# Performance work log

Hardware: AMD Instinct MI355X
Metric: run time of the kernel (lower is better)

The kernel has to match this reference:

```python
import jax, jax.numpy as jnp
import numpy as np

N_NODES = 50000
IN_DIM = 128
HID = 2 * IN_DIM  # 256, per module: hidden_dim = input_dims * 2
FC1 = 1024
FC2 = 512
N_ACT = 64
N_EDGES = 800000
N_AGENTS = 16384


def _layernorm(h, g, b, eps=1e-5):
    mu = jnp.mean(h, axis=-1, keepdims=True)
    var = jnp.var(h, axis=-1, keepdims=True)
    return (h - mu) * jax.lax.rsqrt(var + eps) * g + b


def setup_inputs() -> dict:
    key = jax.random.key(0)
    ks = jax.random.split(key, 16)
    def u(k, shape, fan_in):
        s = 1.0 / np.sqrt(fan_in)
        return jax.random.uniform(k, shape, jnp.float32, -s, s)
    inp = {}
    inp["x"] = jax.random.normal(ks[0], (N_NODES, IN_DIM), jnp.float32)
    inp["action"] = jax.random.normal(ks[1], (N_AGENTS, N_ACT), jnp.float32)
    inp["edge_index"] = jax.random.randint(ks[2], (2, N_EDGES), 0, N_NODES, jnp.int32)
    inp["agent_idx"] = jax.random.randint(ks[3], (N_AGENTS,), 0, N_NODES, jnp.int32)
    # GCNConv params (linear no bias + separate bias)
    inp["W_gcn"] = u(ks[4], (IN_DIM, HID), IN_DIM)
    inp["b_gcn"] = jnp.zeros((HID,), jnp.float32)
    # fc1, fc2 (custom uniform init per module)
    inp["W1"] = u(ks[5], (HID, FC1), FC1)
    inp["b1"] = u(ks[6], (FC1,), FC1)
    inp["g1"] = jnp.ones((FC1,), jnp.float32)
    inp["beta1"] = jnp.zeros((FC1,), jnp.float32)
    inp["W2"] = u(ks[7], (FC1, FC2), FC2)
    inp["b2"] = u(ks[8], (FC2,), FC2)
    inp["g2"] = jnp.ones((FC2,), jnp.float32)
    inp["beta2"] = jnp.zeros((FC2,), jnp.float32)
    inp["Wa"] = u(ks[9], (N_ACT, FC2), FC2)
    inp["ba"] = u(ks[10], (FC2,), FC2)
    inp["Wq"] = jax.random.uniform(ks[11], (FC2, 1), jnp.float32, -0.003, 0.003)
    inp["bq"] = jax.random.uniform(ks[12], (1,), jnp.float32, -0.003, 0.003)
    return inp


def reference(x, action, W_gcn, b_gcn, W1, b1, g1, beta1, W2, b2, g2, beta2, Wa, ba, Wq, bq, edge_index, agent_idx):
    N = x.shape[0]
    # GCNConv: add self-loops, symmetric D^-1/2 (A+I) D^-1/2 normalization
    loops = jnp.arange(N, dtype=edge_index.dtype)
    src = jnp.concatenate([edge_index[0], loops])
    dst = jnp.concatenate([edge_index[1], loops])
    h = x @ W_gcn  # [N, HID] transform before aggregation
    deg = jax.ops.segment_sum(jnp.ones_like(dst, dtype=h.dtype), dst, num_segments=N)
    dinv = jax.lax.rsqrt(jnp.maximum(deg, 1.0))  # deg >= 1 due to self-loops
    norm = dinv[src] * dinv[dst]  # [E+N]
    agg = jax.ops.segment_sum(h[src] * norm[:, None], dst, num_segments=N) + b_gcn
    # masked gather of agent nodes, then critic MLP
    z = jax.nn.relu(agg[agent_idx])  # [A, HID]
    s = jax.nn.relu(_layernorm(z @ W1 + b1, g1, beta1))
    s = _layernorm(s @ W2 + b2, g2, beta2)
    a = action @ Wa + ba
    sa = jax.nn.relu(s + a)
    return sa @ Wq + bq  # [A, 1]
```

## Files before the change

### kernel.cpp

```cpp
#include <hip/hip_runtime.h>
#include <hip/hip_bf16.h>

typedef _Float16 f16;
typedef _Float16 __attribute__((ext_vector_type(8))) half8;
typedef _Float16 __attribute__((ext_vector_type(4))) half4;
typedef float __attribute__((ext_vector_type(4))) floatx4;

#define IN_DIM 128
#define HID    256
#define FC1    1024
#define FC2    512
#define NACT   64
#define BUCKET 128

__global__ void prep0_kernel(int* degcnt, int* needed, int* n_needed, int* cursor, int N, int A) {
    int b = blockIdx.x, tid = threadIdx.x;
    if (b < 196) {
        int i = b * 256 + tid;
        if (i < N) { degcnt[i] = 0; needed[i] = 0; }
        if (b == 0 && tid == 0) *n_needed = 0;
        return;
    }
    b -= 196;
    cursor[b * 256 + tid] = 0;
}

__device__ __forceinline__ void transpose_tile(const float* __restrict__ in, f16* __restrict__ out,
                                               int K, int N, int bx, int by, int tid) {
    __shared__ f16 tile[32][33];
    int k0 = bx * 32, n0 = by * 32;
    int tx = tid & 31, ty = tid >> 5;
    #pragma unroll
    for (int i = 0; i < 4; ++i)
        tile[ty + i * 8][tx] = (f16)in[(size_t)(k0 + ty + i * 8) * N + n0 + tx];
    __syncthreads();
    #pragma unroll
    for (int i = 0; i < 4; ++i)
        out[(size_t)(n0 + ty + i * 8) * K + k0 + tx] = tile[tx][ty + i * 8];
}

__device__ __forceinline__ void cvt8(const float* __restrict__ in, f16* __restrict__ out, long gi) {
    float4 a = *(const float4*)&in[gi * 8];
    float4 b = *(const float4*)&in[gi * 8 + 4];
    half8 pk;
    pk[0] = (f16)a.x; pk[1] = (f16)a.y; pk[2] = (f16)a.z; pk[3] = (f16)a.w;
    pk[4] = (f16)b.x; pk[5] = (f16)b.y; pk[6] = (f16)b.z; pk[7] = (f16)b.w;
    *(half8*)&out[gi * 8] = pk;
}

__global__ __launch_bounds__(256)
void prep1_kernel(const float* __restrict__ Wgcn, const float* __restrict__ W1,
                  const float* __restrict__ W2, const float* __restrict__ Wa,
                  const float* __restrict__ action, const int* __restrict__ agent_idx,
                  f16* WgcnT, f16* W1T, f16* W2T, f16* WaT, f16* act16,
                  int* needed, int* needed_list, int* n_needed, int A) {
    int b = blockIdx.x, tid = threadIdx.x;
    if (b < 32)  { transpose_tile(Wgcn, WgcnT, IN_DIM, HID, b & 3, b >> 2, tid); return; }
    b -= 32;
    if (b < 256) { transpose_tile(W1, W1T, HID, FC1, b & 7, b >> 3, tid); return; }
    b -= 256;
    if (b < 512) { transpose_tile(W2, W2T, FC1, FC2, b & 31, b >> 5, tid); return; }
    b -= 512;
    if (b < 32)  { transpose_tile(Wa, WaT, NACT, FC2, b & 1, b >> 1, tid); return; }
    b -= 32;
    if (b < 512) { cvt8(action, act16, (long)b * 256 + tid); return; }
    b -= 512;
    int i = b * 256 + tid;
    if (i < A) {
        int idx = agent_idx[i];
        if (atomicCAS(&needed[idx], 0, -1) == 0) {
            int p = atomicAdd(n_needed, 1);
            needed_list[p] = idx;
            needed[idx] = p + 1;
        }
    }
}

__device__ __forceinline__ void swz_decode(int bid, int log2ny, int& bx, int& by) {
    int xcd = bid & 7;
    int pos = bid >> 3;
    bx = (pos >> log2ny) * 8 + xcd;
    by = pos & ((1 << log2ny) - 1);
}

template<bool RELU, bool LIMIT>
__device__ __forceinline__ void gemm_tile64(f16* __restrict__ smA, f16* __restrict__ smB,
                                            const f16* __restrict__ A, const f16* __restrict__ BT,
                                            f16* __restrict__ C, const float* __restrict__ bias,
                                            const int* __restrict__ limit,
                                            int bx, int by, int N, int K) {
    if (LIMIT && bx * 64 >= *limit) return;
    const int tid = threadIdx.x;
    const int lane = tid & 63;
    const int wave = tid >> 6;
    const int wr = wave >> 1, wc = wave & 1;
    const long bm = (long)bx * 64, bn = (long)by * 64;

    size_t aoff[2], boff[2];
    #pragma unroll
    for (int t = 0; t < 2; ++t) {
        int ci = t * 256 + tid;
        int r = ci >> 3, s = ci & 7, ks = s ^ (r & 7);
        aoff[t] = (size_t)(bm + r) * K + ks * 8;
        boff[t] = (size_t)(bn + r) * K + ks * 8;
    }
    int aidx[2][2], bidx[2][2];
    const int kc = lane >> 4;
    #pragma unroll
    for (int kk = 0; kk < 2; ++kk) {
        #pragma unroll
        for (int i = 0; i < 2; ++i) {
            int ar = wr * 32 + i * 16 + (lane & 15);
            aidx[kk][i] = ar * 64 + ((kk * 4 + kc) ^ (ar & 7)) * 8;
            int br = wc * 32 + i * 16 + (lane & 15);
            bidx[kk][i] = br * 64 + ((kk * 4 + kc) ^ (br & 7)) * 8;
        }
    }

    const int NT = K >> 6;
    auto stage = [&](int buf, int k0) {
        #pragma unroll
        for (int t = 0; t < 2; ++t) {
            __builtin_amdgcn_global_load_lds(
                (const __attribute__((address_space(1))) void*)(A + aoff[t] + k0),
                (__attribute__((address_space(3))) void*)(&smA[buf * 4096 + (t * 256 + tid) * 8]), 16, 0, 0);
            __builtin_amdgcn_global_load_lds(
                (const __attribute__((address_space(1))) void*)(BT + boff[t] + k0),
                (__attribute__((address_space(3))) void*)(&smB[buf * 4096 + (t * 256 + tid) * 8]), 16, 0, 0);
        }
    };

    floatx4 acc[2][2] = {};
    stage(0, 0);
    asm volatile("s_waitcnt vmcnt(0)" ::: "memory");
    __builtin_amdgcn_s_barrier();
    int cur = 0;
    for (int t = 0; t < NT; ++t) {
        if (t + 1 < NT) stage(cur ^ 1, (t + 1) << 6);
        #pragma unroll
        for (int kk = 0; kk < 2; ++kk) {
            half8 af[2], bf[2];
            #pragma unroll
            for (int i = 0; i < 2; ++i) {
                af[i] = *(const half8*)&smA[cur * 4096 + aidx[kk][i]];
                bf[i] = *(const half8*)&smB[cur * 4096 + bidx[kk][i]];
            }
            #pragma unroll
            for (int mi = 0; mi < 2; ++mi)
                #pragma unroll
                for (int ni = 0; ni < 2; ++ni)
                    acc[mi][ni] = __builtin_amdgcn_mfma_f32_16x16x32_f16(af[mi], bf[ni], acc[mi][ni], 0, 0, 0);
        }
        asm volatile("s_waitcnt vmcnt(0)" ::: "memory");
        __builtin_amdgcn_s_barrier();
        cur ^= 1;
    }
    f16* scr = smA + wave * 512;
    #pragma unroll
    for (int mi = 0; mi < 2; ++mi) {
        __syncthreads();
        #pragma unroll
        for (int ni = 0; ni < 2; ++ni) {
            int c = ni * 16 + (lane & 15);
            float bz = bias[bn + wc * 32 + c];
            #pragma unroll
            for (int q = 0; q < 4; ++q) {
                int r = (lane >> 4) * 4 + q;
                float v = acc[mi][ni][q] + bz;
                if (RELU) v = fmaxf(v, 0.f);
                scr[r * 32 + c] = (f16)v;
            }
        }
        __syncthreads();
        int r = lane >> 2, ch = lane & 3;
        half8 v = *(const half8*)&scr[r * 32 + ch * 8];
        *(half8*)&C[(size_t)(bm + wr * 32 + mi * 16 + r) * N + (bn + wc * 32 + ch * 8)] = v;
    }
}

template<bool RELU, bool LIMIT>
__global__ __launch_bounds__(256)
void gemm64_kernel(const f16* __restrict__ A, const f16* __restrict__ BT,
                   f16* __restrict__ C, const float* __restrict__ bias,
                   const int* __restrict__ limit, int N, int K, int log2ny) {
    __shared__ __align__(16) f16 smA[2 * 4096];
    __shared__ __align__(16) f16 smB[2 * 4096];
    int bx, by;
    swz_decode(blockIdx.x, log2ny, bx, by);
    gemm_tile64<RELU, LIMIT>(smA, smB, A, BT, C, bias, limit, bx, by, N, K);
}

__global__ __launch_bounds__(256)
void degfill_abuf_kernel(const int* __restrict__ esrc, const int* __restrict__ edst,
                         const int* __restrict__ needed, int* __restrict__ degcnt,
                         int* __restrict__ cursor, int* __restrict__ srcbuf,
                         const f16* __restrict__ act16, const f16* __restrict__ WaT,
                         f16* __restrict__ abuf, const float* __restrict__ ba,
                         int E, int gblk) {
    __shared__ __align__(16) f16 smA[2 * 4096];
    __shared__ __align__(16) f16 smB[2 * 4096];
    int b = blockIdx.x;
    if (b < gblk) {
        int bx, by;
        swz_decode(b, 3, bx, by);
        gemm_tile64<false, false>(smA, smB, act16, WaT, abuf, ba, nullptr, bx, by, FC2, NACT);
        return;
    }
    int e = (b - gblk) * 256 + threadIdx.x;
    if (e < E) {
        int d = edst[e];
        int s = needed[d];
        if (s == 0) {
            atomicAdd(&degcnt[d], 1);
        } else {
            int slot = s - 1;
            int pos = atomicAdd(&cursor[slot], 1);
            if (pos < BUCKET) srcbuf[(size_t)slot * BUCKET + pos] = esrc[e];
        }
    }
}

__global__ __launch_bounds__(256)
void gather_x_kernel(const int* __restrict__ needed_list, const int* __restrict__ n_needed,
                     const int* __restrict__ needed, const int* __restrict__ degcnt,
                     const int* __restrict__ cursor, const int* __restrict__ srcbuf,
                     const float* __restrict__ x, f16* __restrict__ xagg) {
    int w = (blockIdx.x * 256 + threadIdx.x) >> 6;
    int lane = threadIdx.x & 63;
    if (w >= *n_needed) return;
    int d = needed_list[w];
    int degd = cursor[w];
    float dd = rsqrtf((float)degd + 1.0f);
    size_t beg = (size_t)w * BUCKET;
    int cnt = degd < BUCKET ? degd : BUCKET;
    float2 xs = *(const float2*)&x[(size_t)d * IN_DIM + lane * 2];
    float ax = xs.x * dd * dd, ay = xs.y * dd * dd;
    auto src_deg = [&](int s) -> float {
        int ns = needed[s];
        int dg = (ns != 0) ? cursor[ns - 1] : degcnt[s];
        return (float)dg;
    };
    int j = 0;
    for (; j + 3 < cnt; j += 4) {
        int s0 = srcbuf[beg + j], s1 = srcbuf[beg + j + 1];
        int s2 = srcbuf[beg + j + 2], s3 = srcbuf[beg + j + 3];
        float n0 = rsqrtf(src_deg(s0) + 1.0f) * dd;
        float n1 = rsqrtf(src_deg(s1) + 1.0f) * dd;
        float n2 = rsqrtf(src_deg(s2) + 1.0f) * dd;
        float n3 = rsqrtf(src_deg(s3) + 1.0f) * dd;
        float2 v0 = *(const float2*)&x[(size_t)s0 * IN_DIM + lane * 2];
        float2 v1 = *(const float2*)&x[(size_t)s1 * IN_DIM + lane * 2];
        float2 v2 = *(const float2*)&x[(size_t)s2 * IN_DIM + lane * 2];
        float2 v3 = *(const float2*)&x[(size_t)s3 * IN_DIM + lane * 2];
        ax = fmaf(v0.x, n0, ax); ay = fmaf(v0.y, n0, ay);
        ax = fmaf(v1.x, n1, ax); ay = fmaf(v1.y, n1, ay);
        ax = fmaf(v2.x, n2, ax); ay = fmaf(v2.y, n2, ay);
        ax = fmaf(v3.x, n3, ax); ay = fmaf(v3.y, n3, ay);
    }
    for (; j < cnt; ++j) {
        int s0 = srcbuf[beg + j];
        float n0 = rsqrtf(src_deg(s0) + 1.0f) * dd;
        float2 v0 = *(const float2*)&x[(size_t)s0 * IN_DIM + lane * 2];
        ax = fmaf(v0.x, n0, ax);
        ay = fmaf(v0.y, n0, ay);
    }
    union { f16 h[2]; unsigned u; } pk;
    pk.h[0] = (f16)ax; pk.h[1] = (f16)ay;
    *(unsigned*)&xagg[(size_t)w * IN_DIM + lane * 2] = pk.u;
}

template<bool LIMIT>
__device__ __forceinline__ void gemm_tile128(f16* __restrict__ smA, f16* __restrict__ smB,
                                             const f16* __restrict__ A, const f16* __restrict__ BT,
                                             f16* __restrict__ C, const float* __restrict__ bias,
                                             const int* __restrict__ limit,
                                             int bx, int by, int N, int K) {
    if (LIMIT && bx * 128 >= *limit) return;
    const int tid = threadIdx.x;
    const int lane = tid & 63;
    const int wave = tid >> 6;
    const int wr = wave >> 1, wc = wave & 1;
    const long bm = (long)bx * 128, bn = (long)by * 128;

    size_t aoff[4], boff[4];
    #pragma unroll
    for (int t = 0; t < 4; ++t) {
        int ci = t * 256 + tid;
        int r = ci >> 3, s = ci & 7, ks = s ^ (r & 7);
        aoff[t] = (size_t)(bm + r) * K + ks * 8;
        boff[t] = (size_t)(bn + r) * K + ks * 8;
    }
    int aidx[2][4], bidx[2][4];
    const int kc = lane >> 4;
    #pragma unroll
    for (int kk = 0; kk < 2; ++kk) {
        #pragma unroll
        for (int i = 0; i < 4; ++i) {
            int ar = wr * 64 + i * 16 + (lane & 15);
            aidx[kk][i] = ar * 64 + ((kk * 4 + kc) ^ (ar & 7)) * 8;
            int br = wc * 64 + i * 16 + (lane & 15);
            bidx[kk][i] = br * 64 + ((kk * 4 + kc) ^ (br & 7)) * 8;
        }
    }

    const int NT = K >> 6;
    auto stage = [&](int buf, int k0) {
        #pragma unroll
        for (int t = 0; t < 4; ++t) {
            __builtin_amdgcn_global_load_lds(
                (const __attribute__((address_space(1))) void*)(A + aoff[t] + k0),
                (__attribute__((address_space(3))) void*)(&smA[buf * 8192 + (t * 256 + tid) * 8]), 16, 0, 0);
            __builtin_amdgcn_global_load_lds(
                (const __attribute__((address_space(1))) void*)(BT + boff[t] + k0),
                (__attribute__((address_space(3))) void*)(&smB[buf * 8192 + (t * 256 + tid) * 8]), 16, 0, 0);
        }
    };

    floatx4 acc[4][4] = {};
    stage(0, 0);
    asm volatile("s_waitcnt vmcnt(0)" ::: "memory");
    __builtin_amdgcn_s_barrier();
    int cur = 0;
    for (int t = 0; t < NT; ++t) {
        if (t + 1 < NT) stage(cur ^ 1, (t + 1) << 6);
        #pragma unroll
        for (int kk = 0; kk < 2; ++kk) {
            half8 af[4], bf[4];
            #pragma unroll
            for (int i = 0; i < 4; ++i) {
                af[i] = *(const half8*)&smA[cur * 8192 + aidx[kk][i]];
                bf[i] = *(const half8*)&smB[cur * 8192 + bidx[kk][i]];
            }
            #pragma unroll
            for (int mi = 0; mi < 4; ++mi)
                #pragma unroll
                for (int ni = 0; ni < 4; ++ni)
                    acc[mi][ni] = __builtin_amdgcn_mfma_f32_16x16x32_f16(af[mi], bf[ni], acc[mi][ni], 0, 0, 0);
        }
        asm volatile("s_waitcnt vmcnt(0)" ::: "memory");
        __builtin_amdgcn_s_barrier();
        cur ^= 1;
    }
    f16* scr = smA + wave * 1024;
    #pragma unroll
    for (int mi = 0; mi < 4; ++mi) {
        __syncthreads();
        #pragma unroll
        for (int ni = 0; ni < 4; ++ni) {
            int c = ni * 16 + (lane & 15);
            float bz = bias[bn + wc * 64 + c];
            #pragma unroll
            for (int q = 0; q < 4; ++q) {
                int r = (lane >> 4) * 4 + q;
                scr[r * 64 + c] = (f16)(acc[mi][ni][q] + bz);
            }
        }
        __syncthreads();
        #pragma unroll
        for (int it = 0; it < 2; ++it) {
            int flat = it * 64 + lane;
            int r = flat >> 3, ch = flat & 7;
            half8 v = *(const half8*)&scr[r * 64 + ch * 8];
            *(half8*)&C[(size_t)(bm + wr * 64 + mi * 16 + r) * N + (bn + wc * 64 + ch * 8)] = v;
        }
    }
}

template<bool LIMIT>
__global__ __launch_bounds__(256)
void gemm128_kernel(const f16* __restrict__ A, const f16* __restrict__ BT,
                    f16* __restrict__ C, const float* __restrict__ bias,
                    const int* __restrict__ limit, int N, int K, int log2ny) {
    __shared__ __align__(16) f16 smA[2 * 8192];
    __shared__ __align__(16) f16 smB[2 * 8192];
    int bx, by;
    swz_decode(blockIdx.x, log2ny, bx, by);
    gemm_tile128<LIMIT>(smA, smB, A, BT, C, bias, limit, bx, by, N, K);
}

__global__ __launch_bounds__(256)
void ln_relu_f16_kernel(f16* __restrict__ s, const float* __restrict__ g,
                        const float* __restrict__ b, const int* __restrict__ nn) {
    int row = blockIdx.x;
    if (row >= *nn) return;
    f16* p = s + (size_t)row * FC1;
    int tid = threadIdx.x;
    half4 v = *(const half4*)&p[tid * 4];
    float f0 = (float)v[0], f1 = (float)v[1], f2 = (float)v[2], f3 = (float)v[3];
    float sum = f0 + f1 + f2 + f3;
    float sq = f0 * f0 + f1 * f1 + f2 * f2 + f3 * f3;
    #pragma unroll
    for (int off = 32; off > 0; off >>= 1) {
        sum += __shfl_down(sum, off);
        sq  += __shfl_down(sq, off);
    }
    __shared__ float ssum[4], ssq[4];
    int wid = tid >> 6;
    if ((tid & 63) == 0) { ssum[wid] = sum; ssq[wid] = sq; }
    __syncthreads();
    float tot = ssum[0] + ssum[1] + ssum[2] + ssum[3];
    float tq  = ssq[0] + ssq[1] + ssq[2] + ssq[3];
    float mu = tot * (1.0f / FC1);
    float var = tq * (1.0f / FC1) - mu * mu;
    float rs = rsqrtf(var + 1e-5f);
    float4 gg = *(const float4*)&g[tid * 4];
    float4 bb = *(const float4*)&b[tid * 4];
    half4 o;
    o[0] = (f16)fmaxf((f0 - mu) * rs * gg.x + bb.x, 0.f);
    o[1] = (f16)fmaxf((f1 - mu) * rs * gg.y + bb.y, 0.f);
    o[2] = (f16)fmaxf((f2 - mu) * rs * gg.z + bb.z, 0.f);
    o[3] = (f16)fmaxf((f3 - mu) * rs * gg.w + bb.w, 0.f);
    *(half4*)&p[tid * 4] = o;
}

__global__ __launch_bounds__(256)
void final_f16_kernel(const f16* __restrict__ s2, const f16* __restrict__ ab,
                      const int* __restrict__ agent_idx, const int* __restrict__ needed,
                      const float* __restrict__ g2, const float* __restrict__ b2,
                      const float* __restrict__ Wq, const float* __restrict__ bq,
                      float* __restrict__ out) {
    int row = blockIdx.x;
    int slot = needed[agent_idx[row]] - 1;
    const f16* p = s2 + (size_t)slot * FC2;
    int tid = threadIdx.x;
    float v0 = (float)p[tid * 2], v1 = (float)p[tid * 2 + 1];
    float sum = v0 + v1;
    float sq = v0 * v0 + v1 * v1;
    #pragma unroll
    for (int off = 32; off > 0; off >>= 1) {
        sum += __shfl_down(sum, off);
        sq  += __shfl_down(sq, off);
    }
    __shared__ float ssum[4], ssq[4], spart[4];
    int wid = tid >> 6;
    if ((tid & 63) == 0) { ssum[wid] = sum; ssq[wid] = sq; }
    __syncthreads();
    float tot = ssum[0] + ssum[1] + ssum[2] + ssum[3];
    float tq  = ssq[0] + ssq[1] + ssq[2] + ssq[3];
    float mu = tot * (1.0f / FC2);
    float var = tq * (1.0f / FC2) - mu * mu;
    float rs = rsqrtf(var + 1e-5f);
    float a0 = (float)ab[(size_t)row * FC2 + tid * 2];
    float a1 = (float)ab[(size_t)row * FC2 + tid * 2 + 1];
    float g0 = g2[tid * 2], g1 = g2[tid * 2 + 1];
    float bb0 = b2[tid * 2], bb1 = b2[tid * 2 + 1];
    float sa0 = fmaxf((v0 - mu) * rs * g0 + bb0 + a0, 0.f);
    float sa1 = fmaxf((v1 - mu) * rs * g1 + bb1 + a1, 0.f);
    float part = sa0 * Wq[tid * 2] + sa1 * Wq[tid * 2 + 1];
    #pragma unroll
    for (int off = 32; off > 0; off >>= 1) part += __shfl_down(part, off);
    if ((tid & 63) == 0) spart[wid] = part;
    __syncthreads();
    if (tid == 0) out[row] = spart[0] + spart[1] + spart[2] + spart[3] + bq[0];
}

extern "C" void kernel_launch(void* const* d_in, const int* in_sizes, int n_in,
                              void* d_out, int out_size, void* d_ws, size_t ws_size,
                              hipStream_t stream) {
    const float* x        = (const float*)d_in[0];
    const float* action   = (const float*)d_in[1];
    const int*   edge     = (const int*)d_in[2];
    const int*   agent_idx= (const int*)d_in[3];
    const float* W_gcn    = (const float*)d_in[4];
    const float* b_gcn    = (const float*)d_in[5];
    const float* W1       = (const float*)d_in[6];
    const float* b1       = (const float*)d_in[7];
    const float* g1       = (const float*)d_in[8];
    const float* beta1    = (const float*)d_in[9];
    const float* W2       = (const float*)d_in[10];
    const float* b2       = (const float*)d_in[11];
    const float* g2       = (const float*)d_in[12];
    const float* beta2    = (const float*)d_in[13];
    const float* Wa       = (const float*)d_in[14];
    const float* ba       = (const float*)d_in[15];
    const float* Wq       = (const float*)d_in[16];
    const float* bq       = (const float*)d_in[17];
    float* out = (float*)d_out;

    const int N = in_sizes[0] / IN_DIM;
    const int E = in_sizes[2] / 2;
    const int A = in_sizes[3];
    const int* esrc = edge;
    const int* edst = edge + E;

    char* ws = (char*)d_ws;
    size_t off = 0;
    auto carve = [&](size_t bytes) -> char* {
        char* p = ws + off;
        off += (bytes + 255) & ~(size_t)255;
        return p;
    };
    int*   degcnt     = (int*)  carve((size_t)N * 4);
    int*   needed     = (int*)  carve((size_t)N * 4);
    int*   cursor     = (int*)  carve((size_t)A * 4);
    int*   needed_list= (int*)  carve((size_t)A * 4);
    int*   n_needed   = (int*)  carve(256);
    int*   srcbuf     = (int*)  carve((size_t)A * BUCKET * 4);
    f16*   WgcnT      = (f16*)  carve((size_t)HID * IN_DIM * 2);
    f16*   W1T        = (f16*)  carve((size_t)FC1 * HID * 2);
    f16*   W2T        = (f16*)  carve((size_t)FC2 * FC1 * 2);
    f16*   WaT        = (f16*)  carve((size_t)FC2 * NACT * 2);
    f16*   act16      = (f16*)  carve((size_t)A * NACT * 2);
    f16*   xagg       = (f16*)  carve((size_t)A * IN_DIM * 2);
    f16*   z          = (f16*)  carve((size_t)A * HID * 2);
    f16*   s1         = (f16*)  carve((size_t)A * FC1 * 2);
    f16*   s2         = (f16*)  carve((size_t)A * FC2 * 2);
    f16*   abuf       = (f16*)  carve((size_t)A * FC2 * 2);
    (void)ws_size;

    const int eblk = (E + 255) / 256;
    const int gblk = (A / 64) * (FC2 / 64);

    prep0_kernel<<<196 + 64, 256, 0, stream>>>(degcnt, needed, n_needed, cursor, N, A);
    prep1_kernel<<<32 + 256 + 512 + 32 + 512 + 64, 256, 0, stream>>>(
        W_gcn, W1, W2, Wa, action, agent_idx,
        WgcnT, W1T, W2T, WaT, act16, needed, needed_list, n_needed, A);
    degfill_abuf_kernel<<<gblk + eblk, 256, 0, stream>>>(
        esrc, edst, needed, degcnt, cursor, srcbuf,
        act16, WaT, abuf, ba, E, gblk);
    gather_x_kernel<<<(A + 3) / 4, 256, 0, stream>>>(needed_list, n_needed, needed,
                                                     degcnt, cursor, srcbuf, x, xagg);
    gemm64_kernel<true, true><<<(A / 64) * (HID / 64), 256, 0, stream>>>(
        xagg, WgcnT, z, b_gcn, n_needed, HID, IN_DIM, 2);
    gemm128_kernel<true><<<(A / 128) * (FC1 / 128), 256, 0, stream>>>(
        z, W1T, s1, b1, n_needed, FC1, HID, 3);
    ln_relu_f16_kernel<<<A, 256, 0, stream>>>(s1, g1, beta1, n_needed);
    gemm128_kernel<true><<<(A / 128) * (FC2 / 128), 256, 0, stream>>>(
        s1, W2T, s2, b2, n_needed, FC2, FC1, 2);
    final_f16_kernel<<<A, 256, 0, stream>>>(s2, abuf, agent_idx, needed, g2, beta2, Wq, bq, out);
}
```

Before: 154.6 us.

## Pre-convert x to fp16 and move weight transposes into the edge-pass kernel

A full fp16 copy of x is now produced inside the combined edge/GEMM kernel. The neighbour gather then reads half-width rows, which halves the bytes of its random-access loads. The GCN, W1 and W2 weight transposes move from prep1 into the same kernel, so they run alongside the edge-counting pass and the action GEMM, leaving prep1 lighter. In exchange, the whole 50000x128 x matrix is read once more and written as fp16, even though only rows near agents are needed. Rounding x to fp16 before aggregation also adds a small precision loss.

```diff
diff --git a/kernel.cpp b/kernel.cpp
--- a/kernel.cpp
+++ b/kernel.cpp
@@ -26,17 +26,17 @@
 }
 
 __device__ __forceinline__ void transpose_tile(const float* __restrict__ in, f16* __restrict__ out,
-                                               int K, int N, int bx, int by, int tid) {
-    __shared__ f16 tile[32][33];
+                                               int K, int N, int bx, int by, int tid,
+                                               f16* __restrict__ tile ) {
     int k0 = bx * 32, n0 = by * 32;
     int tx = tid & 31, ty = tid >> 5;
     #pragma unroll
     for (int i = 0; i < 4; ++i)
-        tile[ty + i * 8][tx] = (f16)in[(size_t)(k0 + ty + i * 8) * N + n0 + tx];
+        tile[(ty + i * 8) * 33 + tx] = (f16)in[(size_t)(k0 + ty + i * 8) * N + n0 + tx];
     __syncthreads();
     #pragma unroll
     for (int i = 0; i < 4; ++i)
-        out[(size_t)(n0 + ty + i * 8) * K + k0 + tx] = tile[tx][ty + i * 8];
+        out[(size_t)(n0 + ty + i * 8) * K + k0 + tx] = tile[tx * 33 + ty + i * 8];
 }
 
 __device__ __forceinline__ void cvt8(const float* __restrict__ in, f16* __restrict__ out, long gi) {
@@ -49,31 +49,28 @@
 }
 
 __global__ __launch_bounds__(256)
-void prep1_kernel(const float* __restrict__ Wgcn, const float* __restrict__ W1,
-                  const float* __restrict__ W2, const float* __restrict__ Wa,
-                  const float* __restrict__ action, const int* __restrict__ agent_idx,
-                  f16* WgcnT, f16* W1T, f16* W2T, f16* WaT, f16* act16,
+void prep1_kernel(const float* __restrict__ Wa, const float* __restrict__ action,
+                  const int* __restrict__ agent_idx,
+                  f16* WaT, f16* act16,
                   int* needed, int* needed_list, int* n_needed, int A) {
+    __shared__ f16 tile[32 * 33];
     int b = blockIdx.x, tid = threadIdx.x;
-    if (b < 32)  { transpose_tile(Wgcn, WgcnT, IN_DIM, HID, b & 3, b >> 2, tid); return; }
+    if (b < 64) {
+        int i = b * 256 + tid;
+        if (i < A) {
+            int idx = agent_idx[i];
+            if (atomicCAS(&needed[idx], 0, -1) == 0) {
+                int p = atomicAdd(n_needed, 1);
+                needed_list[p] = idx;
+                needed[idx] = p + 1;
+            }
+        }
+        return;
+    }
+    b -= 64;
+    if (b < 32) { transpose_tile(Wa, WaT, NACT, FC2, b & 1, b >> 1, tid, tile); return; }
     b -= 32;
-    if (b < 256) { transpose_tile(W1, W1T, HID, FC1, b & 7, b >> 3, tid); return; }
-    b -= 256;
-    if (b < 512) { transpose_tile(W2, W2T, FC1, FC2, b & 31, b >> 5, tid); return; }
-    b -= 512;
-    if (b < 32)  { transpose_tile(Wa, WaT, NACT, FC2, b & 1, b >> 1, tid); return; }
-    b -= 32;
-    if (b < 512) { cvt8(action, act16, (long)b * 256 + tid); return; }
-    b -= 512;
-    int i = b * 256 + tid;
-    if (i < A) {
-        int idx = agent_idx[i];
-        if (atomicCAS(&needed[idx], 0, -1) == 0) {
-            int p = atomicAdd(n_needed, 1);
-            needed_list[p] = idx;
-            needed[idx] = p + 1;
-        }
-    }
+    cvt8(action, act16, (long)b * 256 + tid);
 }
 
 __device__ __forceinline__ void swz_decode(int bid, int log2ny, int& bx, int& by) {
@@ -191,40 +188,56 @@
 }
 
 __global__ __launch_bounds__(256)
-void degfill_abuf_kernel(const int* __restrict__ esrc, const int* __restrict__ edst,
-                         const int* __restrict__ needed, int* __restrict__ degcnt,
-                         int* __restrict__ cursor, int* __restrict__ srcbuf,
-                         const f16* __restrict__ act16, const f16* __restrict__ WaT,
-                         f16* __restrict__ abuf, const float* __restrict__ ba,
-                         int E, int gblk) {
+void mega_kernel(const int* __restrict__ esrc, const int* __restrict__ edst,
+                 const int* __restrict__ needed, int* __restrict__ degcnt,
+                 int* __restrict__ cursor, int* __restrict__ srcbuf,
+                 const f16* __restrict__ act16, const f16* __restrict__ WaT,
+                 f16* __restrict__ abuf, const float* __restrict__ ba,
+                 const float* __restrict__ Wgcn, const float* __restrict__ W1,
+                 const float* __restrict__ W2, const float* __restrict__ x,
+                 f16* WgcnT, f16* W1T, f16* W2T, f16* x16,
+                 int E, int eblk) {
     __shared__ __align__(16) f16 smA[2 * 4096];
     __shared__ __align__(16) f16 smB[2 * 4096];
     int b = blockIdx.x;
-    if (b < gblk) {
+    int tid = threadIdx.x;
+    if (b < eblk) {
+        int e = b * 256 + tid;
+        if (e < E) {
+            int d = edst[e];
+            int s = needed[d];
+            if (s == 0) {
+                atomicAdd(&degcnt[d], 1);
+            } else {
+                int slot = s - 1;
+                int pos = atomicAdd(&cursor[slot], 1);
+                if (pos < BUCKET) srcbuf[(size_t)slot * BUCKET + pos] = esrc[e];
+            }
+        }
+        return;
+    }
+    b -= eblk;
+    if (b < 2048) {
         int bx, by;
         swz_decode(b, 3, bx, by);
         gemm_tile64<false, false>(smA, smB, act16, WaT, abuf, ba, nullptr, bx, by, FC2, NACT);
         return;
     }
-    int e = (b - gblk) * 256 + threadIdx.x;
-    if (e < E) {
-        int d = edst[e];
-        int s = needed[d];
-        if (s == 0) {
-            atomicAdd(&degcnt[d], 1);
-        } else {
-            int slot = s - 1;
-            int pos = atomicAdd(&cursor[slot], 1);
-            if (pos < BUCKET) srcbuf[(size_t)slot * BUCKET + pos] = esrc[e];
-        }
-    }
+    b -= 2048;
+    if (b < 32)  { transpose_tile(Wgcn, WgcnT, IN_DIM, HID, b & 3, b >> 2, tid, smA); return; }
+    b -= 32;
+    if (b < 256) { transpose_tile(W1, W1T, HID, FC1, b & 7, b >> 3, tid, smA); return; }
+    b -= 256;
+    if (b < 512) { transpose_tile(W2, W2T, FC1, FC2, b & 31, b >> 5, tid, smA); return; }
+    b -= 512;
+    cvt8(x, x16, (long)b * 256 + tid);
 }
 
 __global__ __launch_bounds__(256)
 void gather_x_kernel(const int* __restrict__ needed_list, const int* __restrict__ n_needed,
                      const int* __restrict__ needed, const int* __restrict__ degcnt,
                      const int* __restrict__ cursor, const int* __restrict__ srcbuf,
-                     const float* __restrict__ x, f16* __restrict__ xagg) {
+                     const f16* __restrict__ x16, f16* __restrict__ xagg) {
     int w = (blockIdx.x * 256 + threadIdx.x) >> 6;
     int lane = threadIdx.x & 63;
     if (w >= *n_needed) return;
@@ -233,8 +246,9 @@
     float dd = rsqrtf((float)degd + 1.0f);
     size_t beg = (size_t)w * BUCKET;
     int cnt = degd < BUCKET ? degd : BUCKET;
-    float2 xs = *(const float2*)&x[(size_t)d * IN_DIM + lane * 2];
-    float ax = xs.x * dd * dd, ay = xs.y * dd * dd;
+    union { unsigned u; f16 h[2]; } ld0, ld1, ld2, ld3;
+    ld0.u = *(const unsigned*)&x16[(size_t)d * IN_DIM + lane * 2];
+    float ax = (float)ld0.h[0] * dd * dd, ay = (float)ld0.h[1] * dd * dd;
     auto src_deg = [&](int s) -> float {
         int ns = needed[s];
         int dg = (ns != 0) ? cursor[ns - 1] : degcnt[s];
@@ -248,21 +262,21 @@
         float n1 = rsqrtf(src_deg(s1) + 1.0f) * dd;
         float n2 = rsqrtf(src_deg(s2) + 1.0f) * dd;
         float n3 = rsqrtf(src_deg(s3) + 1.0f) * dd;
-        float2 v0 = *(const float2*)&x[(size_t)s0 * IN_DIM + lane * 2];
-        float2 v1 = *(const float2*)&x[(size_t)s1 * IN_DIM + lane * 2];
-        float2 v2 = *(const float2*)&x[(size_t)s2 * IN_DIM + lane * 2];
-        float2 v3 = *(const float2*)&x[(size_t)s3 * IN_DIM + lane * 2];
-        ax = fmaf(v0.x, n0, ax); ay = fmaf(v0.y, n0, ay);
-        ax = fmaf(v1.x, n1, ax); ay = fmaf(v1.y, n1, ay);
-        ax = fmaf(v2.x, n2, ax); ay = fmaf(v2.y, n2, ay);
-        ax = fmaf(v3.x, n3, ax); ay = fmaf(v3.y, n3, ay);
+        ld0.u = *(const unsigned*)&x16[(size_t)s0 * IN_DIM + lane * 2];
+        ld1.u = *(const unsigned*)&x16[(size_t)s1 * IN_DIM + lane * 2];
+        ld2.u = *(const unsigned*)&x16[(size_t)s2 * IN_DIM + lane * 2];
+        ld3.u = *(const unsigned*)&x16[(size_t)s3 * IN_DIM + lane * 2];
+        ax = fmaf((float)ld0.h[0], n0, ax); ay = fmaf((float)ld0.h[1], n0, ay);
+        ax = fmaf((float)ld1.h[0], n1, ax); ay = fmaf((float)ld1.h[1], n1, ay);
+        ax = fmaf((float)ld2.h[0], n2, ax); ay = fmaf((float)ld2.h[1], n2, ay);
+        ax = fmaf((float)ld3.h[0], n3, ax); ay = fmaf((float)ld3.h[1], n3, ay);
     }
     for (; j < cnt; ++j) {
         int s0 = srcbuf[beg + j];
         float n0 = rsqrtf(src_deg(s0) + 1.0f) * dd;
-        float2 v0 = *(const float2*)&x[(size_t)s0 * IN_DIM + lane * 2];
-        ax = fmaf(v0.x, n0, ax);
-        ay = fmaf(v0.y, n0, ay);
+        ld0.u = *(const unsigned*)&x16[(size_t)s0 * IN_DIM + lane * 2];
+        ax = fmaf((float)ld0.h[0], n0, ax);
+        ay = fmaf((float)ld0.h[1], n0, ay);
     }
     union { f16 h[2]; unsigned u; } pk;
     pk.h[0] = (f16)ax; pk.h[1] = (f16)ay;
@@ -501,6 +515,7 @@
     f16*   W2T        = (f16*)  carve((size_t)FC2 * FC1 * 2);
     f16*   WaT        = (f16*)  carve((size_t)FC2 * NACT * 2);
     f16*   act16      = (f16*)  carve((size_t)A * NACT * 2);
+    f16*   x16        = (f16*)  carve((size_t)N * IN_DIM * 2);
     f16*   xagg       = (f16*)  carve((size_t)A * IN_DIM * 2);
     f16*   z          = (f16*)  carve((size_t)A * HID * 2);
     f16*   s1         = (f16*)  carve((size_t)A * FC1 * 2);
@@ -509,17 +524,16 @@
     (void)ws_size;
 
     const int eblk = (E + 255) / 256;
-    const int gblk = (A / 64) * (FC2 / 64);
 
     prep0_kernel<<<196 + 64, 256, 0, stream>>>(degcnt, needed, n_needed, cursor, N, A);
-    prep1_kernel<<<32 + 256 + 512 + 32 + 512 + 64, 256, 0, stream>>>(
-        W_gcn, W1, W2, Wa, action, agent_idx,
-        WgcnT, W1T, W2T, WaT, act16, needed, needed_list, n_needed, A);
-    degfill_abuf_kernel<<<gblk + eblk, 256, 0, stream>>>(
+    prep1_kernel<<<64 + 32 + 512, 256, 0, stream>>>(
+        Wa, action, agent_idx, WaT, act16, needed, needed_list, n_needed, A);
+    mega_kernel<<<eblk + 2048 + 32 + 256 + 512 + eblk, 256, 0, stream>>>(
         esrc, edst, needed, degcnt, cursor, srcbuf,
-        act16, WaT, abuf, ba, E, gblk);
+        act16, WaT, abuf, ba, W_gcn, W1, W2, x,
+        WgcnT, W1T, W2T, x16, E, eblk);
     gather_x_kernel<<<(A + 3) / 4, 256, 0, stream>>>(needed_list, n_needed, needed,
-                                                     degcnt, cursor, srcbuf, x, xagg);
+                                                     degcnt, cursor, srcbuf, x16, xagg);
     gemm64_kernel<true, true><<<(A / 64) * (HID / 64), 256, 0, stream>>>(
         xagg, WgcnT, z, b_gcn, n_needed, HID, IN_DIM, 2);
     gemm128_kernel<true><<<(A / 128) * (FC1 / 128), 256, 0, stream>>>(
```

Result: no change. 156.9 us (+1.5%).
